# Kernel optimization log

Measured on AMD Instinct MI355X. Metric: run time of the kernel, lower is better.

The kernel has to match this reference:

```python
import jax, jax.numpy as jnp
import numpy as np

T, B, D = 512, 16, 128   # cur_seq, batch, d_input
H = 8                    # n_heads
DH = D                   # d_head_inner = d_input in TemporalTX
P = 512                  # prev_seq = hgcn_rollout_len


def setup_inputs() -> dict:
    key = jax.random.key(0)
    ks = jax.random.split(key, 8)
    inp = {
        "inputs": jax.random.normal(ks[0], (T, B, D), jnp.float32),
        "memory": jax.random.normal(ks[1], (2, P, B, D), jnp.float32),  # n_layers+1 = 2
        "w_kv": jax.random.normal(ks[2], (2 * H * DH, D), jnp.float32) * 0.02,
        "w_q": jax.random.normal(ks[3], (H * DH, D), jnp.float32) * 0.02,
        "w_p": jax.random.normal(ks[4], (H * DH, D), jnp.float32) * 0.02,
        "w_out": jax.random.normal(ks[5], (D, H * DH), jnp.float32) * 0.02,
        "u": jax.random.normal(ks[6], (H, DH), jnp.float32) * 0.02,
        "v": jax.random.normal(ks[7], (H, DH), jnp.float32) * 0.02,
    }
    return inp


def _rel_shift(x):
    # x: [I, J, B, H] -> Transformer-XL relative shift
    I, J, b, h = x.shape
    zp = jnp.zeros((I, 1, b, h), x.dtype)
    return jnp.concatenate([zp, x], axis=1).reshape(J + 1, I, b, h)[1:].reshape(I, J, b, h)


def _pos_embs(J, d):
    # positions counting down: J-1 ... 0
    pos = jnp.arange(J - 1, -1, -1, dtype=jnp.float32)
    inv_freq = 1.0 / (10000.0 ** (jnp.arange(0.0, d, 2.0) / d))
    sin_inp = pos[:, None] * inv_freq[None, :]          # [J, d/2]
    return jnp.concatenate([jnp.sin(sin_inp), jnp.cos(sin_inp)], axis=-1)  # [J, d]


def _attention(x, mem, pe, w_kv, w_q, w_p, w_out, u, v, mask):
    cs, bs, _ = x.shape
    J = cs + mem.shape[0]
    xm = jnp.concatenate([mem, x], axis=0)              # [J, B, D]
    kv = jnp.einsum('jbe,fe->jbf', xm, w_kv)            # [J, B, 2*H*DH]
    k, vv = jnp.split(kv, 2, axis=-1)
    k = k.reshape(J, bs, H, DH)
    vv = vv.reshape(J, bs, H, DH)
    q = jnp.einsum('ibe,fe->ibf', x, w_q).reshape(cs, bs, H, DH)
    content = jnp.einsum('ibhd,jbhd->ijbh', q + u, k)   # [I, J, B, H]
    p = jnp.einsum('je,fe->jf', pe, w_p).reshape(J, H, DH)
    position = jnp.einsum('ibhd,jhd->ijbh', q + v, p)
    position = _rel_shift(position)
    attn = content + position
    attn = jnp.where(mask[:, :, None, None], -jnp.inf, attn)
    scale = 1.0 / (DH ** 0.5)
    attn = jax.nn.softmax(attn * scale, axis=1)
    out = jnp.einsum('ijbh,jbhd->ibhd', attn, vv).reshape(cs, bs, H * DH)
    return jnp.einsum('ibf,ef->ibe', out, w_out)        # [I, B, D]


def reference(inputs, memory, w_kv, w_q, w_p, w_out, u, v):
    cs, bs = inputs.shape[:2]
    mem = list(memory)                                   # unbind along layer dim
    ps = mem[0].shape[0]
    J = cs + ps
    mask = jnp.triu(jnp.ones((cs, J), bool), k=1 + ps)   # [cs, J]
    pe = _pos_embs(J, D)                                 # [J, D]
    layer_out = _attention(inputs, mem[0], pe, w_kv, w_q, w_p, w_out, u, v, mask)
    hidden = [inputs, layer_out]
    # update_memory: keep last ps entries of cat(mem, hidden), detached
    new_mem = []
    end = ps + cs
    beg = max(0, end - ps)
    for m, h in zip(mem, hidden):
        cat = jnp.concatenate([m, h], axis=0)
        new_mem.append(jax.lax.stop_gradient(cat[beg:end]))
    return layer_out, jnp.stack(new_mem)
```

## Files before the change

### kernel.cpp

```cpp
#include <hip/hip_runtime.h>


typedef short s16x8 __attribute__((ext_vector_type(8)));
typedef float f32x4 __attribute__((ext_vector_type(4)));

#define MFMA(a, b, c) __builtin_amdgcn_mfma_f32_16x16x32_bf16((a), (b), (c), 0, 0, 0)
#define LDS_FENCE() asm volatile("s_waitcnt lgkmcnt(0)" ::: "memory")

__device__ __forceinline__ unsigned short f2b(float f) {
  unsigned int x = __builtin_bit_cast(unsigned int, f);
  x += 0x7fffu + ((x >> 16) & 1u);
  return (unsigned short)(x >> 16);
}
__device__ __forceinline__ s16x8 ldg8(const unsigned short* p) {
  return *(const s16x8*)p;
}
__device__ __forceinline__ s16x8 ldf8(const float* p) {
  float4 u = ((const float4*)p)[0];
  float4 v = ((const float4*)p)[1];
  s16x8 r;
  r[0] = (short)f2b(u.x); r[1] = (short)f2b(u.y);
  r[2] = (short)f2b(u.z); r[3] = (short)f2b(u.w);
  r[4] = (short)f2b(v.x); r[5] = (short)f2b(v.y);
  r[6] = (short)f2b(v.z); r[7] = (short)f2b(v.w);
  return r;
}
__device__ __forceinline__ void gl2lds(const unsigned short* g, unsigned short* l) {
  __builtin_amdgcn_global_load_lds(
      (const __attribute__((address_space(1))) unsigned int*)(g),
      (__attribute__((address_space(3))) unsigned int*)(l), 16, 0, 0);
}

__global__ __launch_bounds__(256, 2) void k_prep(
    const float* __restrict__ wkv, const float* __restrict__ wq,
    const float* __restrict__ wp, const float* __restrict__ wout,
    unsigned short* __restrict__ wkv_b, unsigned short* __restrict__ wq_b,
    unsigned short* __restrict__ wp_b, unsigned short* __restrict__ wout_b) {
  int id = blockIdx.x * 256 + threadIdx.x;
  const float* src;
  unsigned short* dst;
  int off;
  if (id < 32768) { src = wkv; dst = wkv_b; off = id; }
  else if (id < 49152) { src = wq; dst = wq_b; off = id - 32768; }
  else if (id < 65536) { src = wp; dst = wp_b; off = id - 49152; }
  else { src = wout; dst = wout_b; off = id - 65536; }
  ((s16x8*)dst)[off] = ldf8(src + off * 8);
}

__global__ __launch_bounds__(256, 2) void k_gemm_kv(
    const float* __restrict__ x, const float* __restrict__ mem,
    const unsigned short* __restrict__ wkv_b,
    unsigned short* __restrict__ Kk, unsigned short* __restrict__ Vt) {
  __shared__ float tbuf[4][16][128];
  const int lane = threadIdx.x & 63;
  const int w = threadIdx.x >> 6;
  const int ncg = (blockIdx.x & 3) * 4;
  const int b = (blockIdx.x >> 2) & 15;
  const int jb = (blockIdx.x >> 6) * 128 + w * 32;
  const int l15 = lane & 15, l4 = lane >> 4;

  s16x8 A[2][4];
#pragma unroll
  for (int g = 0; g < 2; ++g) {
    int jr = jb + g * 16 + l15;
    const float* arow =
        (jr < 512 ? mem + (jr * 16 + b) * 128 : x + ((jr - 512) * 16 + b) * 128) + l4 * 8;
    A[g][0] = ldf8(arow); A[g][1] = ldf8(arow + 32);
    A[g][2] = ldf8(arow + 64); A[g][3] = ldf8(arow + 96);
  }

  for (int q = 0; q < 4; ++q) {
    const int nc = ncg + q;
    f32x4 acc[2][8] = {};
#pragma unroll
    for (int fc = 0; fc < 8; ++fc) {
      const unsigned short* brow = wkv_b + (nc * 128 + fc * 16 + l15) * 128 + l4 * 8;
      s16x8 b0 = ldg8(brow), b1 = ldg8(brow + 32), b2 = ldg8(brow + 64), b3 = ldg8(brow + 96);
#pragma unroll
      for (int g = 0; g < 2; ++g) {
        acc[g][fc] = MFMA(A[g][0], b0, acc[g][fc]);
        acc[g][fc] = MFMA(A[g][1], b1, acc[g][fc]);
        acc[g][fc] = MFMA(A[g][2], b2, acc[g][fc]);
        acc[g][fc] = MFMA(A[g][3], b3, acc[g][fc]);
      }
    }

    if (nc < 8) {
#pragma unroll
      for (int g = 0; g < 2; ++g)
#pragma unroll
        for (int fc = 0; fc < 8; ++fc)
#pragma unroll
          for (int r = 0; r < 4; ++r) {
            int j = jb + g * 16 + l4 * 4 + r;
            Kk[((b * 8 + nc) * 1024 + j) * 128 + fc * 16 + l15] = f2b(acc[g][fc][r]);
          }
    } else {
      const int h = nc - 8;
#pragma unroll
      for (int g = 0; g < 2; ++g) {
        LDS_FENCE();
#pragma unroll
        for (int fc = 0; fc < 8; ++fc)
#pragma unroll
          for (int r = 0; r < 4; ++r) tbuf[w][l4 * 4 + r][fc * 16 + l15] = acc[g][fc][r];
        LDS_FENCE();
#pragma unroll
        for (int half = 0; half < 2; ++half) {
          int dd = half * 64 + lane;
          unsigned int wd[8];
#pragma unroll
          for (int pw = 0; pw < 8; ++pw) {
            unsigned int lo = f2b(tbuf[w][2 * pw][dd]);
            unsigned int hi = f2b(tbuf[w][2 * pw + 1][dd]);
            wd[pw] = lo | (hi << 16);
          }
          unsigned short* dst = Vt + ((b * 8 + h) * 128 + dd) * 1024 + jb + g * 16;
          ((uint4*)dst)[0] = make_uint4(wd[0], wd[1], wd[2], wd[3]);
          ((uint4*)dst)[1] = make_uint4(wd[4], wd[5], wd[6], wd[7]);
        }
      }
    }
  }
}

__global__ __launch_bounds__(256, 2) void k_gemm_p(
    const unsigned short* __restrict__ wp_b, unsigned short* __restrict__ Pp) {
  const int lane = threadIdx.x & 63;
  const int w = threadIdx.x >> 6;
  const int nc = blockIdx.x & 7;
  const int c0 = ((blockIdx.x >> 3) * 4 + w) * 16;
  const int l15 = lane & 15, l4 = lane >> 4;

  const float pos = (float)(1023 - (c0 + l15));
  s16x8 a[4];
#pragma unroll
  for (int ks = 0; ks < 4; ++ks)
#pragma unroll
    for (int jj = 0; jj < 8; ++jj) {
      int e = ks * 32 + l4 * 8 + jj;
      int t = e & 63;
      float ang = pos * exp2f(-0.20762050593046014f * (float)t);
      float val = (e < 64) ? sinf(ang) : cosf(ang);
      a[ks][jj] = (short)f2b(val);
    }

  f32x4 acc[8] = {};
#pragma unroll
  for (int fc = 0; fc < 8; ++fc) {
    const unsigned short* brow = wp_b + (nc * 128 + fc * 16 + l15) * 128 + l4 * 8;
    acc[fc] = MFMA(a[0], ldg8(brow), acc[fc]);
    acc[fc] = MFMA(a[1], ldg8(brow + 32), acc[fc]);
    acc[fc] = MFMA(a[2], ldg8(brow + 64), acc[fc]);
    acc[fc] = MFMA(a[3], ldg8(brow + 96), acc[fc]);
  }
#pragma unroll
  for (int fc = 0; fc < 8; ++fc)
#pragma unroll
    for (int r = 0; r < 4; ++r)
      Pp[(nc * 1024 + c0 + l4 * 4 + r) * 128 + fc * 16 + l15] = f2b(acc[fc][r]);
}

__global__ __launch_bounds__(256, 2) void k_flash(
    const float* __restrict__ x, const unsigned short* __restrict__ wq_b,
    const unsigned short* __restrict__ Kk, const unsigned short* __restrict__ Vt,
    const unsigned short* __restrict__ Pp,
    const float* __restrict__ uu, const float* __restrict__ vv,
    unsigned short* __restrict__ OA) {
  __shared__ __align__(16) unsigned short L[37376];
  unsigned short* LK = L;
  unsigned short* LV = L + 8192;
  unsigned short* LP = L + 16384;
  unsigned short* PB = L + 32768;

  const int lane = threadIdx.x & 63;
  const int w = threadIdx.x >> 6;
  const int bh = blockIdx.x & 127;
  const int igw = 7 - (blockIdx.x >> 7);
  const int iw = igw * 64 + w * 16;
  const int b = bh >> 3, h = bh & 7;
  const int l15 = lane & 15, l4 = lane >> 4;
  const int cb4 = 28 - igw * 4;
  const float CSCALE = 0.08838834764831845f * 1.4426950408889634f;

  const unsigned short* K_b = Kk + bh * (1024 * 128);
  const unsigned short* V_b = Vt + bh * (128 * 1024);
  const unsigned short* P_h = Pp + h * (1024 * 128);

  s16x8 qu[4], qv[4];
  {
    const float* arow = x + ((iw + l15) * 16 + b) * 128 + l4 * 8;
    s16x8 a0 = ldf8(arow), a1 = ldf8(arow + 32), a2 = ldf8(arow + 64), a3 = ldf8(arow + 96);
    f32x4 qd[8] = {};
#pragma unroll
    for (int fc = 0; fc < 8; ++fc) {
      const unsigned short* brow = wq_b + (h * 128 + fc * 16 + l15) * 128 + l4 * 8;
      qd[fc] = MFMA(a0, ldg8(brow), qd[fc]);
      qd[fc] = MFMA(a1, ldg8(brow + 32), qd[fc]);
      qd[fc] = MFMA(a2, ldg8(brow + 64), qd[fc]);
      qd[fc] = MFMA(a3, ldg8(brow + 96), qd[fc]);
    }
    unsigned short* qs = LP + w * 2176;
#pragma unroll
    for (int fc = 0; fc < 8; ++fc) {
      float ud = uu[h * 128 + fc * 16 + l15];
#pragma unroll
      for (int r = 0; r < 4; ++r) qs[(l4 * 4 + r) * 136 + fc * 16 + l15] = f2b(qd[fc][r] + ud);
    }
    LDS_FENCE();
#pragma unroll
    for (int ks = 0; ks < 4; ++ks)
      qu[ks] = *(const s16x8*)&qs[l15 * 136 + ks * 32 + l4 * 8];
    LDS_FENCE();
#pragma unroll
    for (int fc = 0; fc < 8; ++fc) {
      float vd = vv[h * 128 + fc * 16 + l15];
#pragma unroll
      for (int r = 0; r < 4; ++r) qs[(l4 * 4 + r) * 136 + fc * 16 + l15] = f2b(qd[fc][r] + vd);
    }
    LDS_FENCE();
#pragma unroll
    for (int ks = 0; ks < 4; ++ks)
      qv[ks] = *(const s16x8*)&qs[l15 * 136 + ks * 32 + l4 * 8];
  }
  __syncthreads();

  f32x4 O[8] = {};
  float rs[4] = {0.f, 0.f, 0.f, 0.f};

  const int tmax = igw + 9;
  for (int t = 0; t < tmax; ++t) {
    const int j0 = t * 64;

#pragma unroll
    for (int q = 0; q < 4; ++q)
      gl2lds(K_b + (j0 + w * 16 + l15) * 128 + q * 32 + l4 * 8, LK + (w * 4 + q) * 512);
#pragma unroll
    for (int q = 0; q < 4; ++q) {
      int m = w * 4 + q, fd = m >> 1, ks = m & 1;
      gl2lds(V_b + (fd * 16 + l15) * 1024 + j0 + ks * 32 + l4 * 8, LV + m * 512);
    }
    if (t == 0) {
#pragma unroll
      for (int q = 0; q < 8; ++q) {
        int m = w * 8 + q, rc = m >> 2, ks = m & 3;
        int gchunk = cb4 + rc, slot = gchunk & 7;
        int grow = gchunk * 16 + l15;
        grow = (grow > 1023) ? 1023 : grow;
        gl2lds(P_h + grow * 128 + ks * 32 + l4 * 8, LP + (slot * 4 + ks) * 512);
      }
    } else {
#pragma unroll
      for (int q = 0; q < 4; ++q) {
        int m = w * 4 + q, gcq = m >> 2, ks = m & 3;
        int gchunk = cb4 + 4 * t + 4 + gcq, slot = gchunk & 7;
        int grow = gchunk * 16 + l15;
        grow = (grow > 1023) ? 1023 : grow;
        gl2lds(P_h + grow * 128 + ks * 32 + l4 * 8, LP + (slot * 4 + ks) * 512);
      }
    }
    __syncthreads();

    f32x4 sc[4];
#pragma unroll
    for (int fc = 0; fc < 4; ++fc) {
      f32x4 t4 = {};
#pragma unroll
      for (int ks = 0; ks < 4; ++ks)
        t4 = MFMA(qu[ks], *(const s16x8*)&LK[(fc * 4 + ks) * 512 + lane * 8], t4);
      sc[fc] = t4;
    }
    f32x4 sp[5];
#pragma unroll
    for (int pc = 0; pc < 5; ++pc) {
      f32x4 t4 = {};
      int slot = (cb4 + 4 * t + 3 - w + pc) & 7;
#pragma unroll
      for (int ks = 0; ks < 4; ++ks)
        t4 = MFMA(qv[ks], *(const s16x8*)&LP[(slot * 4 + ks) * 512 + lane * 8], t4);
      sp[pc] = t4;
    }

    unsigned short* pb = PB + w * 1152;
#pragma unroll
    for (int fc = 0; fc < 4; ++fc)
#pragma unroll
      for (int r = 0; r < 4; ++r) {
        int li = l4 * 4 + r;
        int jj = fc * 16 + l15;
        int cc = jj - li + 15;
        int src = (lane & 48) | (cc & 15);
        float g0 = __shfl(sp[fc][r], src, 64);
        float g1 = __shfl(sp[fc + 1][r], src, 64);
        float pv = ((cc >> 4) == fc) ? g0 : g1;
        float logit = (sc[fc][r] + pv) * CSCALE - 12.0f;
        if (j0 + jj > iw + li + 512) logit = -72.0f;
        float p = exp2f(logit);
        rs[r] += p;
        pb[li * 72 + jj] = f2b(p);
      }

    s16x8 pa0 = *(const s16x8*)&pb[l15 * 72 + l4 * 8];
    s16x8 pa1 = *(const s16x8*)&pb[l15 * 72 + 32 + l4 * 8];
#pragma unroll
    for (int fd = 0; fd < 8; ++fd) {
      O[fd] = MFMA(pa0, *(const s16x8*)&LV[(fd * 2) * 512 + lane * 8], O[fd]);
      O[fd] = MFMA(pa1, *(const s16x8*)&LV[(fd * 2 + 1) * 512 + lane * 8], O[fd]);
    }
    __syncthreads();
  }

  float lrow[4];
#pragma unroll
  for (int r = 0; r < 4; ++r) {
    float s = rs[r];
#pragma unroll
    for (int off = 1; off < 16; off <<= 1) s += __shfl_xor(s, off, 64);
    lrow[r] = s;
  }
#pragma unroll
  for (int fd = 0; fd < 8; ++fd)
#pragma unroll
    for (int r = 0; r < 4; ++r) {
      int li = l4 * 4 + r;
      float o = O[fd][r] / lrow[r];
      OA[((iw + li) * 16 + b) * 1024 + h * 128 + fd * 16 + l15] = f2b(o);
    }
}

__global__ __launch_bounds__(256, 2) void k_out(
    const unsigned short* __restrict__ OA, const unsigned short* __restrict__ wout_b,
    const float* __restrict__ x, float* __restrict__ out) {
  const int lane = threadIdx.x & 63;
  const int w = threadIdx.x >> 6;
  const int half = blockIdx.x & 1;
  const int rt = (blockIdx.x >> 1) * 4 + w;
  const int l15 = lane & 15, l4 = lane >> 4;

  f32x4 acc[4] = {};
  const unsigned short* arow = OA + (rt * 16 + l15) * 1024 + l4 * 8;
#pragma unroll 4
  for (int ks = 0; ks < 32; ++ks) {
    s16x8 a = ldg8(arow + ks * 32);
#pragma unroll
    for (int fc = 0; fc < 4; ++fc) {
      const unsigned short* brow =
          wout_b + (half * 64 + fc * 16 + l15) * 1024 + ks * 32 + l4 * 8;
      acc[fc] = MFMA(a, ldg8(brow), acc[fc]);
    }
  }
#pragma unroll
  for (int fc = 0; fc < 4; ++fc)
#pragma unroll
    for (int r = 0; r < 4; ++r) {
      int rg = rt * 16 + l4 * 4 + r;
      int e = half * 64 + fc * 16 + l15;
      float v = acc[fc][r];
      out[rg * 128 + e] = v;
      out[2097152 + rg * 128 + e] = v;
    }
  const float4* src = (const float4*)(x + rt * 2048 + half * 1024);
  float4* dst = (float4*)(out + 1048576 + rt * 2048 + half * 1024);
  dst[lane] = src[lane];
  dst[64 + lane] = src[64 + lane];
  dst[128 + lane] = src[128 + lane];
  dst[192 + lane] = src[192 + lane];
}

extern "C" void kernel_launch(void* const* d_in, const int* in_sizes, int n_in,
                              void* d_out, int out_size, void* d_ws, size_t ws_size,
                              hipStream_t stream) {
  (void)in_sizes; (void)n_in; (void)out_size; (void)ws_size;
  const float* x    = (const float*)d_in[0];
  const float* mem  = (const float*)d_in[1];
  const float* wkv  = (const float*)d_in[2];
  const float* wq   = (const float*)d_in[3];
  const float* wp   = (const float*)d_in[4];
  const float* wout = (const float*)d_in[5];
  const float* uu   = (const float*)d_in[6];
  const float* vv   = (const float*)d_in[7];
  float* out = (float*)d_out;
  unsigned short* ws = (unsigned short*)d_ws;

  unsigned short* Kk     = ws;
  unsigned short* Vt     = ws + 16777216;
  unsigned short* Pp     = ws + 33554432;
  unsigned short* OA     = ws + 34603008;
  unsigned short* wkv_b  = ws + 42991616;
  unsigned short* wq_b   = ws + 43253760;
  unsigned short* wp_b   = ws + 43384832;
  unsigned short* wout_b = ws + 43515904;

  k_prep<<<320, 256, 0, stream>>>(wkv, wq, wp, wout, wkv_b, wq_b, wp_b, wout_b);
  k_gemm_kv<<<512, 256, 0, stream>>>(x, mem, wkv_b, Kk, Vt);
  k_gemm_p<<<128, 256, 0, stream>>>(wp_b, Pp);
  k_flash<<<1024, 256, 0, stream>>>(x, wq_b, Kk, Vt, Pp, uu, vv, OA);
  k_out<<<256, 256, 0, stream>>>(OA, wout_b, x, out);
}
```

Before: 283.9 us.

## Load positional embeddings directly from global and realign via LDS instead of shuffles

Drops the LDS ring buffer for the projected positional embeddings. Each wave now reads its P rows straight from global memory into the MFMA operands, stages the bf16 position scores in a small per-wave LDS tile, and reads them back at the shifted index, replacing the cross-lane shuffles. The smaller LDS footprint lets launch bounds rise to three blocks per CU for more occupancy. In exchange the position scores are rounded to bf16 before the add, and each wave issues more global loads, some of which hit the same P rows that neighbouring waves also fetch.

```diff
diff --git a/kernel.cpp b/kernel.cpp
--- a/kernel.cpp
+++ b/kernel.cpp
@@ -11,6 +11,10 @@
   unsigned int x = __builtin_bit_cast(unsigned int, f);
   x += 0x7fffu + ((x >> 16) & 1u);
   return (unsigned short)(x >> 16);
+}
+__device__ __forceinline__ float b2f(unsigned short u) {
+  unsigned int t = ((unsigned int)u) << 16;
+  return __builtin_bit_cast(float, t);
 }
 __device__ __forceinline__ s16x8 ldg8(const unsigned short* p) {
   return *(const s16x8*)p;
@@ -161,17 +165,17 @@
       Pp[(nc * 1024 + c0 + l4 * 4 + r) * 128 + fc * 16 + l15] = f2b(acc[fc][r]);
 }
 
-__global__ __launch_bounds__(256, 2) void k_flash(
+__global__ __launch_bounds__(256, 3) void k_flash(
     const float* __restrict__ x, const unsigned short* __restrict__ wq_b,
     const unsigned short* __restrict__ Kk, const unsigned short* __restrict__ Vt,
     const unsigned short* __restrict__ Pp,
     const float* __restrict__ uu, const float* __restrict__ vv,
     unsigned short* __restrict__ OA) {
-  __shared__ __align__(16) unsigned short L[37376];
+  __shared__ __align__(16) unsigned short L[26368];
   unsigned short* LK = L;
   unsigned short* LV = L + 8192;
-  unsigned short* LP = L + 16384;
-  unsigned short* PB = L + 32768;
+  unsigned short* PB = L + 16384;
+  unsigned short* BD = L + 20992;
 
   const int lane = threadIdx.x & 63;
   const int w = threadIdx.x >> 6;
@@ -180,7 +184,6 @@
   const int iw = igw * 64 + w * 16;
   const int b = bh >> 3, h = bh & 7;
   const int l15 = lane & 15, l4 = lane >> 4;
-  const int cb4 = 28 - igw * 4;
   const float CSCALE = 0.08838834764831845f * 1.4426950408889634f;
 
   const unsigned short* K_b = Kk + bh * (1024 * 128);
@@ -200,7 +203,7 @@
       qd[fc] = MFMA(a2, ldg8(brow + 64), qd[fc]);
       qd[fc] = MFMA(a3, ldg8(brow + 96), qd[fc]);
     }
-    unsigned short* qs = LP + w * 2176;
+    unsigned short* qs = L + 16384 + w * 2176;
 #pragma unroll
     for (int fc = 0; fc < 8; ++fc) {
       float ud = uu[h * 128 + fc * 16 + l15];
@@ -231,6 +234,7 @@
   const int tmax = igw + 9;
   for (int t = 0; t < tmax; ++t) {
     const int j0 = t * 64;
+    const int c0w = j0 - iw + 496;
 
 #pragma unroll
     for (int q = 0; q < 4; ++q)
@@ -240,25 +244,6 @@
       int m = w * 4 + q, fd = m >> 1, ks = m & 1;
       gl2lds(V_b + (fd * 16 + l15) * 1024 + j0 + ks * 32 + l4 * 8, LV + m * 512);
     }
-    if (t == 0) {
-#pragma unroll
-      for (int q = 0; q < 8; ++q) {
-        int m = w * 8 + q, rc = m >> 2, ks = m & 3;
-        int gchunk = cb4 + rc, slot = gchunk & 7;
-        int grow = gchunk * 16 + l15;
-        grow = (grow > 1023) ? 1023 : grow;
-        gl2lds(P_h + grow * 128 + ks * 32 + l4 * 8, LP + (slot * 4 + ks) * 512);
-      }
-    } else {
-#pragma unroll
-      for (int q = 0; q < 4; ++q) {
-        int m = w * 4 + q, gcq = m >> 2, ks = m & 3;
-        int gchunk = cb4 + 4 * t + 4 + gcq, slot = gchunk & 7;
-        int grow = gchunk * 16 + l15;
-        grow = (grow > 1023) ? 1023 : grow;
-        gl2lds(P_h + grow * 128 + ks * 32 + l4 * 8, LP + (slot * 4 + ks) * 512);
-      }
-    }
     __syncthreads();
 
     f32x4 sc[4];
@@ -270,15 +255,20 @@
         t4 = MFMA(qu[ks], *(const s16x8*)&LK[(fc * 4 + ks) * 512 + lane * 8], t4);
       sc[fc] = t4;
     }
-    f32x4 sp[5];
+
+    unsigned short* bw = BD + w * 1344;
 #pragma unroll
     for (int pc = 0; pc < 5; ++pc) {
+      int c = c0w + pc * 16 + l15;
+      c = (c > 1023) ? 1023 : c;
+      const unsigned short* pr = P_h + c * 128 + l4 * 8;
       f32x4 t4 = {};
-      int slot = (cb4 + 4 * t + 3 - w + pc) & 7;
-#pragma unroll
-      for (int ks = 0; ks < 4; ++ks)
-        t4 = MFMA(qv[ks], *(const s16x8*)&LP[(slot * 4 + ks) * 512 + lane * 8], t4);
-      sp[pc] = t4;
+      t4 = MFMA(qv[0], ldg8(pr), t4);
+      t4 = MFMA(qv[1], ldg8(pr + 32), t4);
+      t4 = MFMA(qv[2], ldg8(pr + 64), t4);
+      t4 = MFMA(qv[3], ldg8(pr + 96), t4);
+#pragma unroll
+      for (int r = 0; r < 4; ++r) bw[(l4 * 4 + r) * 84 + pc * 16 + l15] = f2b(t4[r]);
     }
 
     unsigned short* pb = PB + w * 1152;
@@ -288,11 +278,7 @@
       for (int r = 0; r < 4; ++r) {
         int li = l4 * 4 + r;
         int jj = fc * 16 + l15;
-        int cc = jj - li + 15;
-        int src = (lane & 48) | (cc & 15);
-        float g0 = __shfl(sp[fc][r], src, 64);
-        float g1 = __shfl(sp[fc + 1][r], src, 64);
-        float pv = ((cc >> 4) == fc) ? g0 : g1;
+        float pv = b2f(bw[li * 84 + (jj - li + 15)]);
         float logit = (sc[fc][r] + pv) * CSCALE - 12.0f;
         if (j0 + jj > iw + li + 512) logit = -72.0f;
         float p = exp2f(logit);
```

After: 373.8 us. 1.32x slower.
